# Optimization experiments

Measured on AMD Instinct MI355X. Metric: run time of the kernel, lower is better.

Reference implementation:

```python
import jax, jax.numpy as jnp
import numpy as np

N_NODES = 50000
N_EDGES = 800000
D_IN = 128
D_OUT = 128


def setup_inputs() -> dict:
    key = jax.random.key(0)
    k1, k2, k3, k4 = jax.random.split(key, 4)
    node_features = jax.random.normal(k1, (N_NODES, D_IN), dtype=jnp.float32)
    edge_index = jax.random.randint(k2, (2, N_EDGES), 0, N_NODES, dtype=jnp.int64)
    # nn.Linear params: weight [out, in], bias [out]
    W = jax.random.normal(k3, (D_OUT, D_IN), dtype=jnp.float32) / np.sqrt(D_IN)
    b = jax.random.normal(k4, (D_OUT,), dtype=jnp.float32) * 0.01
    return {"node_features": node_features, "edge_index": edge_index, "W": W, "b": b}


def reference(node_features, edge_index, W, b):
    source_nodes = edge_index[0]
    dest_nodes = edge_index[1]
    # gather neighbor features [E, D_in], scatter-add into [N, D_in]
    neighbor_features = node_features[source_nodes]
    aggregated = jax.ops.segment_sum(neighbor_features, dest_nodes,
                                     num_segments=node_features.shape[0])
    # nn.Linear: x @ W.T + b
    return aggregated @ W.T + b
```

## Files before the change

kernel.cpp:

```cpp
#include <hip/hip_runtime.h>


constexpr int NN = 50000;
constexpr int NE = 800000;
constexpr int D  = 128;

constexpr int BS   = 32;
constexpr int NB   = (NN + BS - 1) / BS;
constexpr int EPB  = 4096;
constexpr int NSB  = (NE + EPB - 1) / EPB;
constexpr int CAP  = 1024;

constexpr int AROWU = 136;

typedef __attribute__((ext_vector_type(8))) short bf16x8;
typedef __attribute__((ext_vector_type(4))) float f32x4;
typedef __attribute__((ext_vector_type(2))) float f32x2;

__device__ inline unsigned short f2bf(float f) {
    unsigned u = __float_as_uint(f);
    return (unsigned short)((u + 0x7fffu + ((u >> 16) & 1u)) >> 16);
}
__device__ inline float bflo(unsigned v) { return __uint_as_float(v << 16); }
__device__ inline float bfhi(unsigned v) { return __uint_as_float(v & 0xffff0000u); }

__device__ inline int wscan(int v) {
    #pragma unroll
    for (int o = 1; o < 64; o <<= 1) {
        int u = __shfl_up(v, o);
        if ((int)(threadIdx.x & 63) >= o) v += u;
    }
    return v;
}

__device__ inline void acc8(f32x2& a0, f32x2& a1, f32x2& a2, f32x2& a3, uint4 v) {
    a0 += (f32x2){bflo(v.x), bfhi(v.x)};
    a1 += (f32x2){bflo(v.y), bfhi(v.y)};
    a2 += (f32x2){bflo(v.z), bfhi(v.z)};
    a3 += (f32x2){bflo(v.w), bfhi(v.w)};
}

constexpr int NF4 = NN * D / 4;
constexpr int W4  = D * D / 4;
constexpr int NBLK_P = (NF4 + W4 + 511) / 512;
constexpr int GRID_A = NSB + NBLK_P;

__global__ __launch_bounds__(512) void k_prep_bucket(
    const float* __restrict__ nf, const float* __restrict__ W,
    const int* __restrict__ ei,
    ushort* __restrict__ nfh, ushort* __restrict__ Wh,
    ushort* __restrict__ offs, unsigned* __restrict__ buf)
{
    __shared__ int hist[NB], cur[NB];
    __shared__ int wsum[8];
    __shared__ unsigned spk[EPB];
    const int t = threadIdx.x, lane = t & 63, w = t >> 6;

    if (blockIdx.x < NSB) {
        const int blk = blockIdx.x;
        const int e0  = blk * EPB;
        int cnt = NE - e0; if (cnt > EPB) cnt = EPB;

        for (int i = t; i < NB; i += 512) hist[i] = 0;
        __syncthreads();

        unsigned pk[8];
        #pragma unroll
        for (int j = 0; j < 8; ++j) {
            int idx = j * 512 + t;
            if (idx < cnt) {
                int e = e0 + idx;
                unsigned s = (unsigned)ei[e];
                unsigned d = (unsigned)ei[NE + e];
                pk[j] = (d << 16) | s;
                atomicAdd(&hist[pk[j] >> 21], 1);
            }
        }
        __syncthreads();
        const int base = 4 * t;
        int h0 = (base     < NB) ? hist[base]     : 0;
        int h1 = (base + 1 < NB) ? hist[base + 1] : 0;
        int h2 = (base + 2 < NB) ? hist[base + 2] : 0;
        int h3 = (base + 3 < NB) ? hist[base + 3] : 0;
        int s4 = h0 + h1 + h2 + h3;
        int v = wscan(s4);
        if (lane == 63) wsum[w] = v;
        __syncthreads();
        int addv = 0;
        #pragma unroll
        for (int i = 0; i < 8; ++i) addv += (i < w) ? wsum[i] : 0;
        v += addv;
        int e0b = v - s4, e1b = e0b + h0, e2b = e1b + h1, e3b = e2b + h2;
        if (base     < NB) { cur[base]     = e0b; offs[(base    ) * NSB + blk] = (ushort)e0b; }
        if (base + 1 < NB) { cur[base + 1] = e1b; offs[(base + 1) * NSB + blk] = (ushort)e1b; }
        if (base + 2 < NB) { cur[base + 2] = e2b; offs[(base + 2) * NSB + blk] = (ushort)e2b; }
        if (base + 3 < NB) { cur[base + 3] = e3b; offs[(base + 3) * NSB + blk] = (ushort)e3b; }
        if (t == 0) offs[NB * NSB + blk] = (ushort)cnt;
        __syncthreads();
        #pragma unroll
        for (int j = 0; j < 8; ++j) {
            int idx = j * 512 + t;
            if (idx < cnt) {
                int l = atomicAdd(&cur[pk[j] >> 21], 1);
                spk[l] = pk[j];
            }
        }
        __syncthreads();
        for (int i = t; i < cnt; i += 512)
            buf[(size_t)blk * EPB + i] = spk[i];
    } else {
        int i = (blockIdx.x - NSB) * 512 + t;
        if (i < NF4) {
            float4 v = ((const float4*)nf)[i];
            ((ushort4*)nfh)[i] = make_ushort4(f2bf(v.x), f2bf(v.y), f2bf(v.z), f2bf(v.w));
        } else if (i < NF4 + W4) {
            int k = i - NF4;
            float4 v = ((const float4*)W)[k];
            ((ushort4*)Wh)[k] = make_ushort4(f2bf(v.x), f2bf(v.y), f2bf(v.z), f2bf(v.w));
        }
    }
}

__global__ __launch_bounds__(512) void k_sort_agg(
    const unsigned* __restrict__ nfh, const unsigned* __restrict__ buf,
    const ushort* __restrict__ offs, const ushort* __restrict__ Wh,
    const float* __restrict__ bias, float* __restrict__ out)
{
    __shared__ ushort srt[CAP];
    __shared__ int scnt[256];
    __shared__ int sbase[NSB], rbase[NSB];
    __shared__ int hist[BS], off[BS], cur[BS];
    __shared__ int wred[16];
    __shared__ __align__(16) unsigned tile[BS * AROWU / 2];
    const int b = blockIdx.x, t = threadIdx.x;
    const int lane = t & 63, w = t >> 6;

    int my = 0;
    if (t < NSB) {
        int o0 = (int)offs[b * NSB + t];
        int o1 = (int)offs[(b + 1) * NSB + t];
        rbase[t] = o0;
        my = o1 - o0;
    }
    if (t < BS) hist[t] = 0;
    int vs = 0;
    if (w < 4) {
        vs = wscan(my);
        if (lane == 63) wred[w] = vs;
    }
    __syncthreads();
    if (w < 4) {
        int addv = 0;
        #pragma unroll
        for (int i = 0; i < 3; ++i) addv += (i < w) ? wred[i] : 0;
        vs += addv;
        scnt[t] = vs;
        if (t < NSB) sbase[t] = vs - my;
    }
    __syncthreads();
    int total = scnt[NSB - 1];
    if (total > CAP) total = CAP;

    unsigned mypk[2];
    int mycnt = 0;
    #pragma unroll
    for (int j = 0; j < 2; ++j) {
        int p = t + j * 512;
        if (p < total) {
            int lo = 0, hi = NSB - 1;
            while (lo < hi) {
                int mid = (lo + hi) >> 1;
                if (scnt[mid] > p) hi = mid; else lo = mid + 1;
            }
            unsigned pk = buf[(size_t)lo * EPB + rbase[lo] + (p - sbase[lo])];
            mypk[j] = pk;
            atomicAdd(&hist[(pk >> 16) & (BS - 1)], 1);
            mycnt = j + 1;
        }
    }
    __syncthreads();

    int hv = (t < BS) ? hist[t] : 0;
    int nv = 0;
    if (w == 0) nv = wscan(hv);
    __syncthreads();
    if (t < BS) { int ex = nv - hv; off[t] = ex; cur[t] = ex; }
    __syncthreads();
    #pragma unroll
    for (int j = 0; j < 2; ++j) {
        if (j < mycnt) {
            unsigned pk = mypk[j];
            int n = (pk >> 16) & (BS - 1);
            int p = atomicAdd(&cur[n], 1);
            srt[p] = (ushort)(pk & 0xffffu);
        }
    }
    __syncthreads();

    const int qq = lane >> 4;
    const int sl = lane & 15;
    const uint4* nfv = (const uint4*)nfh;

    {
        const int n = w * 4 + qq;
        const int beg = off[n], cnt = hist[n];
        f32x2 a0 = {0.f, 0.f}, a1 = {0.f, 0.f}, a2 = {0.f, 0.f}, a3 = {0.f, 0.f};
        int p = 0;
        for (; p + 2 <= cnt; p += 2) {
            const int s0 = srt[beg + p];
            const int s1 = srt[beg + p + 1];
            const uint4 v0 = nfv[(size_t)s0 * 16 + sl];
            const uint4 v1 = nfv[(size_t)s1 * 16 + sl];
            acc8(a0, a1, a2, a3, v0);
            acc8(a0, a1, a2, a3, v1);
        }
        if (p < cnt) {
            const int s0 = srt[beg + p];
            const uint4 v0 = nfv[(size_t)s0 * 16 + sl];
            acc8(a0, a1, a2, a3, v0);
        }
        uint4 o;
        o.x = (unsigned)f2bf(a0.x) | ((unsigned)f2bf(a0.y) << 16);
        o.y = (unsigned)f2bf(a1.x) | ((unsigned)f2bf(a1.y) << 16);
        o.z = (unsigned)f2bf(a2.x) | ((unsigned)f2bf(a2.y) << 16);
        o.w = (unsigned)f2bf(a3.x) | ((unsigned)f2bf(a3.y) << 16);
        *(uint4*)(tile + n * (AROWU / 2) + sl * 4) = o;
    }
    __syncthreads();

    const int m = lane & 15, q = lane >> 4;
    const ushort* lds = (const ushort*)tile;
    #pragma unroll
    for (int i = 0; i < 2; ++i) {
        const int task = w + 8 * i;
        const int t16  = task >> 3;
        const int c0   = (task & 7) * 16;
        const int grow0 = b * BS + t16 * 16;
        if (grow0 < NN) {
            bf16x8 a[4];
            const ushort* arow = lds + (t16 * 16 + m) * AROWU + q * 8;
            #pragma unroll
            for (int kk = 0; kk < 4; ++kk)
                a[kk] = *(const bf16x8*)(arow + kk * 32);
            float bv = bias[c0 + m];
            f32x4 acc4 = { bv, bv, bv, bv };
            const ushort* wrow = Wh + (size_t)(c0 + m) * D + q * 8;
            #pragma unroll
            for (int kk = 0; kk < 4; ++kk) {
                bf16x8 bb = *(const bf16x8*)(wrow + kk * 32);
                acc4 = __builtin_amdgcn_mfma_f32_16x16x32_bf16(a[kk], bb, acc4, 0, 0, 0);
            }
            float* op = out + (size_t)(grow0 + q * 4) * D + c0 + m;
            op[0]     = acc4[0];
            op[D]     = acc4[1];
            op[2 * D] = acc4[2];
            op[3 * D] = acc4[3];
        }
    }
}

extern "C" void kernel_launch(void* const* d_in, const int* in_sizes, int n_in,
                              void* d_out, int out_size, void* d_ws, size_t ws_size,
                              hipStream_t stream) {
    const float* nf = (const float*)d_in[0];
    const int*   ei = (const int*)d_in[1];
    const float* W  = (const float*)d_in[2];
    const float* b  = (const float*)d_in[3];
    float* out = (float*)d_out;

    ushort*   nfh  = (ushort*)d_ws;
    ushort*   Wh   = nfh + (size_t)NN * D;
    unsigned* buf  = (unsigned*)(Wh + D * D);
    ushort*   offs = (ushort*)(buf + (size_t)NSB * EPB);

    k_prep_bucket<<<GRID_A, 512, 0, stream>>>(nf, W, ei, nfh, Wh, offs, buf);
    k_sort_agg   <<<NB, 512, 0, stream>>>((const unsigned*)nfh, buf, offs, Wh, b, out);
}
```

Before: 128.5 us.

## Pipeline neighbor gathers through LDS with async global_load_lds and wave reductions

Replaces the per-lane register gather loop with a software pipeline per wave. Up to three chunks of eight neighbor rows are loaded asynchronously into a four-slot LDS staging buffer using global_load_lds, with explicit vmcnt waits. Each lane accumulates part of a row from LDS, and partial sums are combined with cross-lane shuffles. The aim is more memory-level parallelism in the latency-bound gather. The cost is 64KB of extra LDS per block, which can lower occupancy, plus added shuffle reduction work and more complex wait control.

After: 161.1 us. 25.4% more time.

```diff
diff --git a/kernel.cpp b/kernel.cpp
--- a/kernel.cpp
+++ b/kernel.cpp
@@ -23,6 +23,9 @@
 }
 __device__ inline float bflo(unsigned v) { return __uint_as_float(v << 16); }
 __device__ inline float bfhi(unsigned v) { return __uint_as_float(v & 0xffff0000u); }
+__device__ inline unsigned pk2(f32x2 a) {
+    return (unsigned)f2bf(a.x) | ((unsigned)f2bf(a.y) << 16);
+}
 
 __device__ inline int wscan(int v) {
     #pragma unroll
@@ -33,12 +36,23 @@
     return v;
 }
 
-__device__ inline void acc8(f32x2& a0, f32x2& a1, f32x2& a2, f32x2& a3, uint4 v) {
-    a0 += (f32x2){bflo(v.x), bfhi(v.x)};
-    a1 += (f32x2){bflo(v.y), bfhi(v.y)};
-    a2 += (f32x2){bflo(v.z), bfhi(v.z)};
-    a3 += (f32x2){bflo(v.w), bfhi(v.w)};
-}
+__device__ inline void red3(f32x2& a) {
+    a.x += __shfl_xor(a.x, 8);  a.y += __shfl_xor(a.y, 8);
+    a.x += __shfl_xor(a.x, 16); a.y += __shfl_xor(a.y, 16);
+    a.x += __shfl_xor(a.x, 32); a.y += __shfl_xor(a.y, 32);
+}
+
+__device__ __forceinline__ void gl_lds16(const unsigned* g, unsigned* l) {
+    __builtin_amdgcn_global_load_lds(
+        (const __attribute__((address_space(1))) unsigned*)g,
+        (__attribute__((address_space(3))) unsigned*)l, 16, 0, 0);
+}
+#define WAITVM4() { asm volatile("s_waitcnt vmcnt(4)" ::: "memory"); \
+                    __builtin_amdgcn_sched_barrier(0); }
+#define WAITVM2() { asm volatile("s_waitcnt vmcnt(2)" ::: "memory"); \
+                    __builtin_amdgcn_sched_barrier(0); }
+#define WAITVM0() { asm volatile("s_waitcnt vmcnt(0)" ::: "memory"); \
+                    __builtin_amdgcn_sched_barrier(0); }
 
 constexpr int NF4 = NN * D / 4;
 constexpr int W4  = D * D / 4;
@@ -132,6 +146,7 @@
     __shared__ int hist[BS], off[BS], cur[BS];
     __shared__ int wred[16];
     __shared__ __align__(16) unsigned tile[BS * AROWU / 2];
+    __shared__ __align__(16) unsigned stag[8][2048];
     const int b = blockIdx.x, t = threadIdx.x;
     const int lane = t & 63, w = t >> 6;
 
@@ -197,34 +212,81 @@
     }
     __syncthreads();
 
-    const int qq = lane >> 4;
-    const int sl = lane & 15;
-    const uint4* nfv = (const uint4*)nfh;
-
-    {
-        const int n = w * 4 + qq;
-        const int beg = off[n], cnt = hist[n];
-        f32x2 a0 = {0.f, 0.f}, a1 = {0.f, 0.f}, a2 = {0.f, 0.f}, a3 = {0.f, 0.f};
-        int p = 0;
-        for (; p + 2 <= cnt; p += 2) {
-            const int s0 = srt[beg + p];
-            const int s1 = srt[beg + p + 1];
-            const uint4 v0 = nfv[(size_t)s0 * 16 + sl];
-            const uint4 v1 = nfv[(size_t)s1 * 16 + sl];
-            acc8(a0, a1, a2, a3, v0);
-            acc8(a0, a1, a2, a3, v1);
-        }
-        if (p < cnt) {
-            const int s0 = srt[beg + p];
-            const uint4 v0 = nfv[(size_t)s0 * 16 + sl];
-            acc8(a0, a1, a2, a3, v0);
-        }
-        uint4 o;
-        o.x = (unsigned)f2bf(a0.x) | ((unsigned)f2bf(a0.y) << 16);
-        o.y = (unsigned)f2bf(a1.x) | ((unsigned)f2bf(a1.y) << 16);
-        o.z = (unsigned)f2bf(a2.x) | ((unsigned)f2bf(a2.y) << 16);
-        o.w = (unsigned)f2bf(a3.x) | ((unsigned)f2bf(a3.y) << 16);
-        *(uint4*)(tile + n * (AROWU / 2) + sl * 4) = o;
+    const int qq = lane >> 4, sl = lane & 15;
+    const int eL = lane >> 3, dL = lane & 7;
+    const unsigned* nfu = nfh;
+    unsigned* stagw = stag[w];
+    const int wn0 = w * 4;
+
+    int is_n = 0, is_c = 0, fi_issue = 0;
+    auto adv = [&]() {
+        while (is_n < 4) {
+            int ct = hist[wn0 + is_n];
+            if (is_c < ((ct + 7) >> 3)) break;
+            ++is_n; is_c = 0;
+        }
+    };
+    auto issue1 = [&]() {
+        const int beg = off[wn0 + is_n];
+        const int lim = beg + hist[wn0 + is_n] - 1;
+        unsigned* dst = stagw + (fi_issue & 3) * 512;
+        #pragma unroll
+        for (int j = 0; j < 2; ++j) {
+            const int ec = 4 * j + qq;
+            int e = beg + is_c * 8 + ec;
+            if (e > lim) e = lim;
+            const int gslot = sl ^ (ec << 1);
+            gl_lds16(nfu + (size_t)srt[e] * 64 + gslot * 4, dst + j * 256);
+        }
+        ++fi_issue; ++is_c; adv();
+    };
+    adv();
+    if (is_n < 4) issue1();
+    if (is_n < 4) issue1();
+    if (is_n < 4) issue1();
+
+    int fi = 0;
+    #pragma unroll 1
+    for (int n = 0; n < 4; ++n) {
+        f32x2 a0 = {0.f,0.f}, a1 = {0.f,0.f}, a2 = {0.f,0.f}, a3 = {0.f,0.f};
+        f32x2 a4 = {0.f,0.f}, a5 = {0.f,0.f}, a6 = {0.f,0.f}, a7 = {0.f,0.f};
+        const int cnt = hist[wn0 + n];
+        const int nc = (cnt + 7) >> 3;
+        #pragma unroll 1
+        for (int c = 0; c < nc; ++c, ++fi) {
+            const int ahead = fi_issue - fi;
+            if (ahead >= 3)      WAITVM4()
+            else if (ahead == 2) WAITVM2()
+            else                 WAITVM0()
+            if (is_n < 4) issue1();
+            const int ro  = (fi & 3) * 512 + eL * 64 + ((dL ^ eL) << 3);
+            const int par = (eL & 1) << 2;
+            uint4 xa = *(const uint4*)(stagw + ro + par);
+            uint4 xb = *(const uint4*)(stagw + ro + 4 - par);
+            uint4 lo = (eL & 1) ? xb : xa;
+            uint4 hi = (eL & 1) ? xa : xb;
+            int kmax = cnt - 8 * c; if (kmax > 8) kmax = 8;
+            if (eL < kmax) {
+                a0 += (f32x2){bflo(lo.x), bfhi(lo.x)};
+                a1 += (f32x2){bflo(lo.y), bfhi(lo.y)};
+                a2 += (f32x2){bflo(lo.z), bfhi(lo.z)};
+                a3 += (f32x2){bflo(lo.w), bfhi(lo.w)};
+                a4 += (f32x2){bflo(hi.x), bfhi(hi.x)};
+                a5 += (f32x2){bflo(hi.y), bfhi(hi.y)};
+                a6 += (f32x2){bflo(hi.z), bfhi(hi.z)};
+                a7 += (f32x2){bflo(hi.w), bfhi(hi.w)};
+            }
+        }
+        red3(a0); red3(a1); red3(a2); red3(a3);
+        red3(a4); red3(a5); red3(a6); red3(a7);
+        if (lane < 8) {
+            unsigned* tr = tile + (wn0 + n) * (AROWU / 2) + lane * 8;
+            uint4 o1, o2;
+            o1.x = pk2(a0); o1.y = pk2(a1); o1.z = pk2(a2); o1.w = pk2(a3);
+            o2.x = pk2(a4); o2.y = pk2(a5); o2.z = pk2(a6); o2.w = pk2(a7);
+            *(uint4*)tr = o1;
+            *(uint4*)(tr + 4) = o2;
+        }
     }
     __syncthreads();
 
```
